# Performance work log

Measured on AMD Instinct MI355X. Metric: run time of the kernel, lower is better.

## Reference

```python
import jax, jax.numpy as jnp
import numpy as np

D_MODEL, D_INNER, D_STATE, DT_RANK, D_CONV = 1024, 2048, 16, 64, 4
B, L = 2, 2048


def setup_inputs() -> dict:
    key = jax.random.key(0)
    ks = jax.random.split(key, 14)
    s = lambda k, shp, fan: jax.random.normal(k, shp, jnp.float32) / np.sqrt(fan)
    return {
        "resid": jax.random.normal(ks[0], (B, L, D_MODEL), jnp.float32),
        "norm_w": jnp.ones((D_MODEL,), jnp.float32),
        "skip_w": s(ks[1], (D_INNER, D_MODEL), D_MODEL),
        "in_w": s(ks[2], (D_INNER, D_MODEL), D_MODEL),
        "conv_w": s(ks[3], (D_INNER, D_CONV), D_CONV),
        "conv_b": jnp.zeros((D_INNER,), jnp.float32),
        "wd1": s(ks[4], (DT_RANK, D_INNER), D_INNER),
        "wd2": s(ks[5], (D_INNER, DT_RANK), DT_RANK),
        "wd2_b": jnp.zeros((D_INNER,), jnp.float32),
        "wb": s(ks[6], (D_STATE, D_INNER), D_INNER),
        "wc": s(ks[7], (D_STATE, D_INNER), D_INNER),
        "A_log": jax.random.normal(ks[8], (D_INNER, D_STATE), jnp.float32),
        "W_D": jnp.ones((D_INNER,), jnp.float32),
        "out_w": s(ks[9], (D_MODEL, D_INNER), D_INNER),
    }


def _rmsnorm(x, w, eps=1e-5):
    return x * jax.lax.rsqrt(jnp.mean(x * x, axis=-1, keepdims=True) + eps) * w


def _causal_depthwise_conv(x, conv_w, conv_b):
    # x: (B, L, E); conv_w: (E, K). Torch Conv1d padding=K-1 then slice [:L] == causal left pad.
    K = conv_w.shape[1]
    xp = jnp.pad(x, ((0, 0), (K - 1, 0), (0, 0)))
    Lx = x.shape[1]
    out = conv_b
    for k in range(K):
        out = out + xp[:, k:k + Lx, :] * conv_w[:, k]
    return out


def _selective_scan(x, delta, Bm, Cm, A):
    # x, delta: (B, L, E); Bm, Cm: (B, L, N); A: (E, N)
    h0 = jnp.zeros((x.shape[0], A.shape[0], A.shape[1]), x.dtype)

    def step(h, inp):
        xt, dt, bt, ct = inp  # (B,E), (B,E), (B,N), (B,N)
        A_bar = jnp.exp(dt[..., None] * A)                      # (B,E,N)
        h = A_bar * h + (dt * xt)[..., None] * bt[:, None, :]   # (B,E,N)
        y = jnp.einsum('ben,bn->be', h, ct)
        return h, y

    xs = tuple(jnp.swapaxes(a, 0, 1) for a in (x, delta, Bm, Cm))
    _, ys = jax.lax.scan(step, h0, xs)
    return jnp.swapaxes(ys, 0, 1)  # (B, L, E)


def reference(resid, norm_w, skip_w, in_w, conv_w, conv_b, wd1, wd2, wd2_b, wb, wc, A_log, W_D, out_w):
    x = _rmsnorm(resid, norm_w)
    skip = x @ skip_w.T                       # (B,L,E)
    x = x @ in_w.T                            # (B,L,E)
    x = _causal_depthwise_conv(x, conv_w, conv_b)
    x = jax.nn.silu(x)
    A = -jnp.exp(A_log)                       # (E,N)
    delta = jax.nn.softplus((x @ wd1.T) @ wd2.T + wd2_b)  # (B,L,E)
    Bm = x @ wb.T                             # (B,L,N)
    Cm = x @ wc.T                             # (B,L,N)
    y = _selective_scan(x, delta, Bm, Cm, A)
    y = y + x * W_D
    y = y * jax.nn.silu(skip)
    y = y @ out_w.T                           # (B,L,D)
    return resid + y
```

## Files before the change

kernel.cpp:

```cpp
#include <hip/hip_runtime.h>
#include <stdint.h>

typedef unsigned short u16;
typedef unsigned int u32;
typedef __bf16 bf16x8 __attribute__((ext_vector_type(8)));
typedef u16 u16x8 __attribute__((ext_vector_type(8)));
typedef float f32x4 __attribute__((ext_vector_type(4)));

#define LOG2E 1.44269504088896340736f

__device__ __forceinline__ u16 f2bf(float f) {
  u32 u = __float_as_uint(f);
  u += 0x7fffu + ((u >> 16) & 1u);
  return (u16)(u >> 16);
}
__device__ __forceinline__ float bf2f(u16 s) { return __uint_as_float(((u32)s) << 16); }
__device__ __forceinline__ float fexp2(float x) { return __builtin_amdgcn_exp2f(x); }

struct alignas(8) U16x4 { u16 x, y, z, w; };

__device__ __forceinline__ void load_lds16(const u16* g, u16* l) {
  __builtin_amdgcn_global_load_lds((const __attribute__((address_space(1))) void*)g,
                                   (__attribute__((address_space(3))) void*)l, 16, 0, 0);
}

struct CvtArgs {
  const float* src[8];
  u16* dst[8];
  int cnt4[8];
  int total4;
};

__global__ __launch_bounds__(256) void cvt8_kernel(CvtArgs a) {
  for (int g = blockIdx.x * 256 + threadIdx.x; g < a.total4; g += gridDim.x * 256) {
    int i = 0, off = g;
    while (off >= a.cnt4[i]) { off -= a.cnt4[i]; ++i; }
    float4 v = make_float4(0.f, 0.f, 0.f, 0.f);
    if (a.src[i]) v = ((const float4*)a.src[i])[off];
    U16x4 o;
    o.x = f2bf(v.x); o.y = f2bf(v.y); o.z = f2bf(v.z); o.w = f2bf(v.w);
    ((U16x4*)a.dst[i])[off] = o;
  }
}

__global__ __launch_bounds__(256) void cvt_t96_kernel(const float* __restrict__ src,
                                                      u16* __restrict__ dst) {
  const int g = blockIdx.x * 256 + threadIdx.x;
  const float4 v = ((const float4*)src)[g];
  U16x4 o;
  o.x = f2bf(v.x); o.y = f2bf(v.y); o.z = f2bf(v.z); o.w = f2bf(v.w);
  ((U16x4*)dst)[g] = o;
}

__global__ __launch_bounds__(256) void rmsnorm_kernel(const float* __restrict__ resid,
                                                      const float* __restrict__ w,
                                                      u16* __restrict__ xn) {
  const int row = blockIdx.x;
  const int tid = threadIdx.x;
  const float4 v = ((const float4*)(resid + (size_t)row * 1024))[tid];
  float ss = v.x * v.x + v.y * v.y + v.z * v.z + v.w * v.w;
#pragma unroll
  for (int off = 32; off > 0; off >>= 1) ss += __shfl_down(ss, off, 64);
  __shared__ float red[4];
  const int lane = tid & 63, wid = tid >> 6;
  if (lane == 0) red[wid] = ss;
  __syncthreads();
  const float tot = red[0] + red[1] + red[2] + red[3];
  const float sc = rsqrtf(tot * (1.0f / 1024.0f) + 1e-5f);
  const float4 wv = ((const float4*)w)[tid];
  U16x4 o;
  o.x = f2bf(v.x * sc * wv.x); o.y = f2bf(v.y * sc * wv.y);
  o.z = f2bf(v.z * sc * wv.z); o.w = f2bf(v.w * sc * wv.w);
  ((U16x4*)(xn + (size_t)row * 1024))[tid] = o;
}

template <int EPI>
__global__ __launch_bounds__(256) void gemm_bt(
    const u16* __restrict__ A, const u16* __restrict__ Bw,
    void* __restrict__ C1, void* __restrict__ C2,
    const float* __restrict__ bias, const float* __restrict__ resid,
    int Kslice, int lda, int ldb, int ldc, int split, int nstore) {
  __shared__ alignas(16) u16 As[2][128 * 32];
  __shared__ alignas(16) u16 Bs[2][128 * 32];
  const int tid = threadIdx.x;
  const int lane = tid & 63, wid = tid >> 6;
  const int wr = wid >> 1, wcid = wid & 1;

  int bx, by;
  {
    const int gy = gridDim.y;
    const int flat = blockIdx.y * 32 + blockIdx.x;
    if ((gy & 3) == 0) {
      const int xcd = flat & 7, idx = flat >> 3;
      const int sy = gy >> 2;
      bx = (xcd & 1) * 16 + (idx & 15);
      by = (xcd >> 1) * sy + (idx >> 4);
    } else { bx = blockIdx.x; by = blockIdx.y; }
  }

  const long brow = (long)bx * 128, bcol = (long)by * 128;
  const int kt0 = blockIdx.z * Kslice;
  const int nt = Kslice >> 5;

  f32x4 acc[4][4] = {};

  const int srow = tid >> 2;
  const int scol = ((tid & 3) ^ ((srow >> 1) & 3)) * 8;
  const u16* Ag = A + (brow + srow) * (long)lda + scol;
  const u16* Bg = Bw + (bcol + srow) * (long)ldb + scol;
  const int fr = lane & 15;
  const int kk2 = ((lane >> 4) ^ ((lane >> 1) & 3)) * 8;

  {
    u16* Asp = As[0] + tid * 8;
    u16* Bsp = Bs[0] + tid * 8;
    load_lds16(Ag + kt0, Asp);
    load_lds16(Ag + kt0 + 64L * lda, Asp + 64 * 32);
    load_lds16(Bg + kt0, Bsp);
    load_lds16(Bg + kt0 + 64L * ldb, Bsp + 64 * 32);
  }
  __syncthreads();

  int cur = 0;
  for (int t = 0; t < nt; ++t) {
    if (t + 1 < nt) {
      const int kt = kt0 + (t + 1) * 32;
      u16* Asp = As[cur ^ 1] + tid * 8;
      u16* Bsp = Bs[cur ^ 1] + tid * 8;
      load_lds16(Ag + kt, Asp);
      load_lds16(Ag + kt + 64L * lda, Asp + 64 * 32);
      load_lds16(Bg + kt, Bsp);
      load_lds16(Bg + kt + 64L * ldb, Bsp + 64 * 32);
    }
    bf16x8 af[4], bfr[4];
#pragma unroll
    for (int i = 0; i < 4; ++i) {
      af[i]  = *(const bf16x8*)(As[cur] + (wr * 64 + i * 16 + fr) * 32 + kk2);
      bfr[i] = *(const bf16x8*)(Bs[cur] + (wcid * 64 + i * 16 + fr) * 32 + kk2);
    }
#pragma unroll
    for (int i = 0; i < 4; ++i)
#pragma unroll
      for (int j = 0; j < 4; ++j)
        acc[i][j] = __builtin_amdgcn_mfma_f32_16x16x32_bf16(af[i], bfr[j], acc[i][j], 0, 0, 0);
    if (t + 1 < nt) __syncthreads();
    cur ^= 1;
  }

  const int fq = lane >> 4;
#pragma unroll
  for (int i = 0; i < 4; ++i) {
#pragma unroll
    for (int j = 0; j < 4; ++j) {
      const long col = bcol + wcid * 64 + j * 16 + fr;
      if ((int)col < nstore) {
#pragma unroll
        for (int r = 0; r < 4; ++r) {
          const long row = brow + wr * 64 + i * 16 + fq * 4 + r;
          float v = acc[i][j][r];
          if (EPI == 1) {
            v += bias[col];
            v = fmaxf(v, 0.f) + log1pf(__expf(-fabsf(v)));
          }
          if (EPI == 4) {
            atomicAdd((float*)C1 + row * ldc + col, v);
          } else if (EPI == 2) {
            ((float*)C1)[row * ldc + col] = v + resid[row * ldc + col];
          } else if ((int)col < split) {
            ((u16*)C1)[row * ldc + col] = f2bf(v);
          } else {
            ((u16*)C2)[row * ldc + (col - split)] = f2bf(v);
          }
        }
      }
    }
  }
}

__global__ __launch_bounds__(256) void conv_silu_kernel(
    const u16* __restrict__ u, const float* __restrict__ cw, const float* __restrict__ cb,
    u16* __restrict__ xc) {
  const int row = blockIdx.x;
  const int l = row & 2047;
  const int t = threadIdx.x;
  const int e0 = t * 8;
  const size_t base = (size_t)row * 2048 + e0;
  bf16x8 xv[4];
#pragma unroll
  for (int k = 0; k < 4; ++k) {
    const int ls = l - 3 + k;
    if (ls >= 0) xv[k] = *(const bf16x8*)(u + base + (long)(k - 3) * 2048);
    else { bf16x8 z = {}; xv[k] = z; }
  }
  u16x8 o;
#pragma unroll
  for (int j = 0; j < 8; ++j) {
    const int e = e0 + j;
    const float4 w = ((const float4*)cw)[e];
    float acc = cb[e];
    acc = fmaf(w.x, (float)xv[0][j], acc);
    acc = fmaf(w.y, (float)xv[1][j], acc);
    acc = fmaf(w.z, (float)xv[2][j], acc);
    acc = fmaf(w.w, (float)xv[3][j], acc);
    const float s = acc / (1.f + __expf(-acc));
    o[j] = f2bf(s);
  }
  *(u16x8*)(xc + base) = o;
}

__global__ __launch_bounds__(256) void scan_p1(
    const u16* __restrict__ delta, const u16* __restrict__ xc, const u16* __restrict__ t96,
    const float* __restrict__ A_log, float* __restrict__ P, float* __restrict__ H) {
  const int tid = threadIdx.x;
  const int e = blockIdx.x * 256 + tid;
  const int c = blockIdx.y, b = blockIdx.z;
  __shared__ alignas(16) u16 Dsh[32 * 256];
  __shared__ alignas(16) u16 Xsh[32 * 256];
  __shared__ float Bsh[32][16];
  const size_t rowbase = ((size_t)(b * 2048 + c * 32)) * 2048 + blockIdx.x * 256;
#pragma unroll
  for (int k = 0; k < 4; ++k) {
    const int i = tid + k * 256;
    const size_t go = rowbase + (size_t)(i >> 5) * 2048 + (i & 31) * 8;
    load_lds16(delta + go, Dsh + i * 8);
    load_lds16(xc + go, Xsh + i * 8);
  }
  for (int i = tid; i < 512; i += 256) {
    const int l0 = i >> 4, n = i & 15;
    Bsh[l0][n] = bf2f(t96[(size_t)(b * 2048 + c * 32 + l0) * 96 + 64 + n]);
  }
  float kv[16], h[16];
#pragma unroll
  for (int n = 0; n < 16; ++n) {
    kv[n] = -__expf(A_log[(size_t)e * 16 + n]) * LOG2E;
    h[n] = 0.f;
  }
  __syncthreads();
  float sdt = 0.f;
  for (int l0 = 0; l0 < 32; ++l0) {
    const float dt = bf2f(Dsh[l0 * 256 + tid]);
    const float x  = bf2f(Xsh[l0 * 256 + tid]);
    const float dtx = dt * x;
    sdt += dt;
#pragma unroll
    for (int n = 0; n < 16; ++n) {
      const float ab = fexp2(kv[n] * dt);
      h[n] = fmaf(ab, h[n], dtx * Bsh[l0][n]);
    }
  }
  const size_t o0 = (((size_t)(b * 64 + c)) * 16) * 2048 + e;
#pragma unroll
  for (int n = 0; n < 16; ++n) {
    P[o0 + (size_t)n * 2048] = fexp2(kv[n] * sdt);
    H[o0 + (size_t)n * 2048] = h[n];
  }
}

__global__ __launch_bounds__(256) void scan_p2(float* __restrict__ P, float* __restrict__ H) {
  const int g = blockIdx.x * 256 + threadIdx.x;
  const int e = g & 2047;
  const int n = (g >> 11) & 15;
  const int b = g >> 15;
  const size_t base = (((size_t)(b * 64)) * 16 + n) * 2048 + e;
  float h = 0.f;
  for (int c = 0; c < 64; ++c) {
    const size_t a = base + (size_t)c * (16 * 2048);
    const float Pc = P[a], hl = H[a];
    H[a] = h;
    h = fmaf(Pc, h, hl);
  }
}

__global__ __launch_bounds__(256) void scan_p3(
    const u16* __restrict__ delta, const u16* __restrict__ xc, const u16* __restrict__ t96,
    const float* __restrict__ A_log, const float* __restrict__ Hin,
    const u16* __restrict__ skip, const float* __restrict__ W_D, u16* __restrict__ ybar) {
  const int tid = threadIdx.x;
  const int e = blockIdx.x * 256 + tid;
  const int c = blockIdx.y, b = blockIdx.z;
  __shared__ alignas(16) u16 Dsh[32 * 256];
  __shared__ alignas(16) u16 Xsh[32 * 256];
  __shared__ float Bsh[32][16], Csh[32][16];
  const size_t rowbase = ((size_t)(b * 2048 + c * 32)) * 2048 + blockIdx.x * 256;
#pragma unroll
  for (int k = 0; k < 4; ++k) {
    const int i = tid + k * 256;
    const size_t go = rowbase + (size_t)(i >> 5) * 2048 + (i & 31) * 8;
    load_lds16(delta + go, Dsh + i * 8);
    load_lds16(xc + go, Xsh + i * 8);
  }
  for (int i = tid; i < 512; i += 256) {
    const int l0 = i >> 4, n = i & 15;
    const size_t rowo = (size_t)(b * 2048 + c * 32 + l0) * 96;
    Bsh[l0][n] = bf2f(t96[rowo + 64 + n]);
    Csh[l0][n] = bf2f(t96[rowo + 80 + n]);
  }
  float kv[16], h[16];
  const size_t o0 = (((size_t)(b * 64 + c)) * 16) * 2048 + e;
#pragma unroll
  for (int n = 0; n < 16; ++n) {
    kv[n] = -__expf(A_log[(size_t)e * 16 + n]) * LOG2E;
    h[n] = Hin[o0 + (size_t)n * 2048];
  }
  const float wd = W_D[e];
  __syncthreads();
  const size_t base = ((size_t)(b * 2048 + c * 32)) * 2048 + e;
  for (int l0 = 0; l0 < 32; ++l0) {
    const float dt = bf2f(Dsh[l0 * 256 + tid]);
    const float x  = bf2f(Xsh[l0 * 256 + tid]);
    const float dtx = dt * x;
    float y = 0.f;
#pragma unroll
    for (int n = 0; n < 16; ++n) {
      const float ab = fexp2(kv[n] * dt);
      h[n] = fmaf(ab, h[n], dtx * Bsh[l0][n]);
      y = fmaf(h[n], Csh[l0][n], y);
    }
    y = fmaf(x, wd, y);
    const float s = bf2f(skip[base + (size_t)l0 * 2048]);
    y *= s / (1.f + __expf(-s));
    ybar[base + (size_t)l0 * 2048] = f2bf(y);
  }
}

extern "C" void kernel_launch(void* const* d_in, const int* in_sizes, int n_in,
                              void* d_out, int out_size, void* d_ws, size_t ws_size,
                              hipStream_t stream) {
  const float* resid  = (const float*)d_in[0];
  const float* norm_w = (const float*)d_in[1];
  const float* skip_w = (const float*)d_in[2];
  const float* in_w   = (const float*)d_in[3];
  const float* conv_w = (const float*)d_in[4];
  const float* conv_b = (const float*)d_in[5];
  const float* wd1    = (const float*)d_in[6];
  const float* wd2    = (const float*)d_in[7];
  const float* wd2_b  = (const float*)d_in[8];
  const float* wb     = (const float*)d_in[9];
  const float* wc     = (const float*)d_in[10];
  const float* A_log  = (const float*)d_in[11];
  const float* W_D    = (const float*)d_in[12];
  const float* out_w  = (const float*)d_in[13];
  float* out = (float*)d_out;

  char* ws = (char*)d_ws;
  u16* w_in   = (u16*)(ws + 0);
  u16* w_skip = (u16*)(ws + 4194304);
  u16* w_out  = (u16*)(ws + 8388608);
  u16* w_wd2  = (u16*)(ws + 12582912);
  u16* w2cat  = (u16*)(ws + 12845056);
  u16* xn     = (u16*)(ws + 13369344);
  u16* u      = (u16*)(ws + 21757952);
  u16* delta  = u;
  u16* skip   = (u16*)(ws + 38535168);
  u16* xc     = (u16*)(ws + 55312384);
  u16* t96    = (u16*)(ws + 72089600);
  float* P    = (float*)(ws + 72876032);
  float* t96f = (float*)(ws + 72876032);
  u16* ybar   = (u16*)(ws + 72876032);
  float* H    = (float*)(ws + 89653248);

  CvtArgs ca{};
  ca.src[0] = in_w;   ca.dst[0] = w_in;              ca.cnt4[0] = 2097152 / 4;
  ca.src[1] = skip_w; ca.dst[1] = w_skip;            ca.cnt4[1] = 2097152 / 4;
  ca.src[2] = out_w;  ca.dst[2] = w_out;             ca.cnt4[2] = 2097152 / 4;
  ca.src[3] = wd2;    ca.dst[3] = w_wd2;             ca.cnt4[3] = 131072 / 4;
  ca.src[4] = wd1;    ca.dst[4] = w2cat;             ca.cnt4[4] = 131072 / 4;
  ca.src[5] = wb;     ca.dst[5] = w2cat + 64 * 2048; ca.cnt4[5] = 32768 / 4;
  ca.src[6] = wc;     ca.dst[6] = w2cat + 80 * 2048; ca.cnt4[6] = 32768 / 4;
  ca.src[7] = nullptr;ca.dst[7] = w2cat + 96 * 2048; ca.cnt4[7] = 65536 / 4;
  ca.total4 = (2097152 * 3 + 131072 * 2 + 32768 * 2 + 65536) / 4;
  cvt8_kernel<<<2048, 256, 0, stream>>>(ca);

  rmsnorm_kernel<<<4096, 256, 0, stream>>>(resid, norm_w, xn);

  gemm_bt<0><<<dim3(32, 32), 256, 0, stream>>>(xn, w_in, u, skip, nullptr, nullptr,
                                               1024, 1024, 1024, 2048, 2048, 4096);

  conv_silu_kernel<<<4096, 256, 0, stream>>>(u, conv_w, conv_b, xc);

  hipMemsetAsync(t96f, 0, 4096 * 96 * 4, stream);
  gemm_bt<4><<<dim3(32, 1, 4), 256, 0, stream>>>(xc, w2cat, t96f, nullptr, nullptr, nullptr,
                                                 512, 2048, 2048, 96, 1 << 30, 96);
  cvt_t96_kernel<<<384, 256, 0, stream>>>(t96f, t96);

  gemm_bt<1><<<dim3(32, 16), 256, 0, stream>>>(t96, w_wd2, delta, nullptr, wd2_b, nullptr,
                                               64, 96, 64, 2048, 1 << 30, 2048);

  scan_p1<<<dim3(8, 64, 2), 256, 0, stream>>>(delta, xc, t96, A_log, P, H);
  scan_p2<<<256, 256, 0, stream>>>(P, H);
  scan_p3<<<dim3(8, 64, 2), 256, 0, stream>>>(delta, xc, t96, A_log, H, skip, W_D, ybar);

  gemm_bt<2><<<dim3(32, 8), 256, 0, stream>>>(ybar, w_out, out, nullptr, nullptr, resid,
                                              2048, 2048, 2048, 1024, 1 << 30, 1024);
}
```

Baseline: 345.0 us.

## Double GEMM K-tile to 64 with new LDS swizzle and fuse prep kernels

The bf16 GEMM now stages a 64-wide K slice per iteration instead of 32. It uses an 8-chunk XOR swizzle and issues two MFMA sub-steps per barrier, which halves the number of sync/load rounds. The weight conversion and RMSNorm kernels are merged into one launch that splits work by block index, saving a launch and letting both run concurrently. The cost is double the LDS per block (64KB), which may lower occupancy.

```diff
diff --git a/kernel.cpp b/kernel.cpp
--- a/kernel.cpp
+++ b/kernel.cpp
@@ -31,15 +31,38 @@
   int total4;
 };
 
-__global__ __launch_bounds__(256) void cvt8_kernel(CvtArgs a) {
-  for (int g = blockIdx.x * 256 + threadIdx.x; g < a.total4; g += gridDim.x * 256) {
-    int i = 0, off = g;
-    while (off >= a.cnt4[i]) { off -= a.cnt4[i]; ++i; }
-    float4 v = make_float4(0.f, 0.f, 0.f, 0.f);
-    if (a.src[i]) v = ((const float4*)a.src[i])[off];
+__global__ __launch_bounds__(256) void prep_kernel(CvtArgs a,
+                                                   const float* __restrict__ resid,
+                                                   const float* __restrict__ w,
+                                                   u16* __restrict__ xn) {
+  const int tid = threadIdx.x;
+  if (blockIdx.x < 4096) {
+    const int row = blockIdx.x;
+    const float4 v = ((const float4*)(resid + (size_t)row * 1024))[tid];
+    float ss = v.x * v.x + v.y * v.y + v.z * v.z + v.w * v.w;
+#pragma unroll
+    for (int off = 32; off > 0; off >>= 1) ss += __shfl_down(ss, off, 64);
+    __shared__ float red[4];
+    const int lane = tid & 63, wid = tid >> 6;
+    if (lane == 0) red[wid] = ss;
+    __syncthreads();
+    const float tot = red[0] + red[1] + red[2] + red[3];
+    const float sc = rsqrtf(tot * (1.0f / 1024.0f) + 1e-5f);
+    const float4 wv = ((const float4*)w)[tid];
     U16x4 o;
-    o.x = f2bf(v.x); o.y = f2bf(v.y); o.z = f2bf(v.z); o.w = f2bf(v.w);
-    ((U16x4*)a.dst[i])[off] = o;
+    o.x = f2bf(v.x * sc * wv.x); o.y = f2bf(v.y * sc * wv.y);
+    o.z = f2bf(v.z * sc * wv.z); o.w = f2bf(v.w * sc * wv.w);
+    ((U16x4*)(xn + (size_t)row * 1024))[tid] = o;
+  } else {
+    for (int g = (blockIdx.x - 4096) * 256 + tid; g < a.total4; g += 2048 * 256) {
+      int i = 0, off = g;
+      while (off >= a.cnt4[i]) { off -= a.cnt4[i]; ++i; }
+      float4 v = make_float4(0.f, 0.f, 0.f, 0.f);
+      if (a.src[i]) v = ((const float4*)a.src[i])[off];
+      U16x4 o;
+      o.x = f2bf(v.x); o.y = f2bf(v.y); o.z = f2bf(v.z); o.w = f2bf(v.w);
+      ((U16x4*)a.dst[i])[off] = o;
+    }
   }
 }
 
@@ -52,36 +75,14 @@
   ((U16x4*)dst)[g] = o;
 }
 
-__global__ __launch_bounds__(256) void rmsnorm_kernel(const float* __restrict__ resid,
-                                                      const float* __restrict__ w,
-                                                      u16* __restrict__ xn) {
-  const int row = blockIdx.x;
-  const int tid = threadIdx.x;
-  const float4 v = ((const float4*)(resid + (size_t)row * 1024))[tid];
-  float ss = v.x * v.x + v.y * v.y + v.z * v.z + v.w * v.w;
-#pragma unroll
-  for (int off = 32; off > 0; off >>= 1) ss += __shfl_down(ss, off, 64);
-  __shared__ float red[4];
-  const int lane = tid & 63, wid = tid >> 6;
-  if (lane == 0) red[wid] = ss;
-  __syncthreads();
-  const float tot = red[0] + red[1] + red[2] + red[3];
-  const float sc = rsqrtf(tot * (1.0f / 1024.0f) + 1e-5f);
-  const float4 wv = ((const float4*)w)[tid];
-  U16x4 o;
-  o.x = f2bf(v.x * sc * wv.x); o.y = f2bf(v.y * sc * wv.y);
-  o.z = f2bf(v.z * sc * wv.z); o.w = f2bf(v.w * sc * wv.w);
-  ((U16x4*)(xn + (size_t)row * 1024))[tid] = o;
-}
-
 template <int EPI>
 __global__ __launch_bounds__(256) void gemm_bt(
     const u16* __restrict__ A, const u16* __restrict__ Bw,
     void* __restrict__ C1, void* __restrict__ C2,
     const float* __restrict__ bias, const float* __restrict__ resid,
     int Kslice, int lda, int ldb, int ldc, int split, int nstore) {
-  __shared__ alignas(16) u16 As[2][128 * 32];
-  __shared__ alignas(16) u16 Bs[2][128 * 32];
+  __shared__ alignas(16) u16 As[2][128 * 64];
+  __shared__ alignas(16) u16 Bs[2][128 * 64];
   const int tid = threadIdx.x;
   const int lane = tid & 63, wid = tid >> 6;
   const int wr = wid >> 1, wcid = wid & 1;
@@ -100,54 +101,54 @@
 
   const long brow = (long)bx * 128, bcol = (long)by * 128;
   const int kt0 = blockIdx.z * Kslice;
-  const int nt = Kslice >> 5;
+  const int nt = Kslice >> 6;
 
   f32x4 acc[4][4] = {};
 
-  const int srow = tid >> 2;
-  const int scol = ((tid & 3) ^ ((srow >> 1) & 3)) * 8;
+  const int srow = tid >> 3;
+  const int scol = ((tid & 7) ^ (srow & 7)) * 8;
   const u16* Ag = A + (brow + srow) * (long)lda + scol;
   const u16* Bg = Bw + (bcol + srow) * (long)ldb + scol;
   const int fr = lane & 15;
-  const int kk2 = ((lane >> 4) ^ ((lane >> 1) & 3)) * 8;
-
-  {
-    u16* Asp = As[0] + tid * 8;
-    u16* Bsp = Bs[0] + tid * 8;
-    load_lds16(Ag + kt0, Asp);
-    load_lds16(Ag + kt0 + 64L * lda, Asp + 64 * 32);
-    load_lds16(Bg + kt0, Bsp);
-    load_lds16(Bg + kt0 + 64L * ldb, Bsp + 64 * 32);
-  }
+  const int fq = lane >> 4;
+  const int ck0 = ((fq) ^ (fr & 7)) * 8;
+  const int ck1 = ((4 + fq) ^ (fr & 7)) * 8;
+
+  auto stage = [&](int buf, int kt) {
+    u16* Asp = As[buf] + tid * 8;
+    u16* Bsp = Bs[buf] + tid * 8;
+#pragma unroll
+    for (int kq = 0; kq < 4; ++kq) {
+      load_lds16(Ag + kt + (long)(kq * 32) * lda, Asp + kq * 2048);
+      load_lds16(Bg + kt + (long)(kq * 32) * ldb, Bsp + kq * 2048);
+    }
+  };
+
+  stage(0, kt0);
   __syncthreads();
 
   int cur = 0;
   for (int t = 0; t < nt; ++t) {
-    if (t + 1 < nt) {
-      const int kt = kt0 + (t + 1) * 32;
-      u16* Asp = As[cur ^ 1] + tid * 8;
-      u16* Bsp = Bs[cur ^ 1] + tid * 8;
-      load_lds16(Ag + kt, Asp);
-      load_lds16(Ag + kt + 64L * lda, Asp + 64 * 32);
-      load_lds16(Bg + kt, Bsp);
-      load_lds16(Bg + kt + 64L * ldb, Bsp + 64 * 32);
-    }
-    bf16x8 af[4], bfr[4];
-#pragma unroll
-    for (int i = 0; i < 4; ++i) {
-      af[i]  = *(const bf16x8*)(As[cur] + (wr * 64 + i * 16 + fr) * 32 + kk2);
-      bfr[i] = *(const bf16x8*)(Bs[cur] + (wcid * 64 + i * 16 + fr) * 32 + kk2);
-    }
-#pragma unroll
-    for (int i = 0; i < 4; ++i)
-#pragma unroll
-      for (int j = 0; j < 4; ++j)
-        acc[i][j] = __builtin_amdgcn_mfma_f32_16x16x32_bf16(af[i], bfr[j], acc[i][j], 0, 0, 0);
+    if (t + 1 < nt) stage(cur ^ 1, kt0 + (t + 1) * 64);
+#pragma unroll
+    for (int ks = 0; ks < 2; ++ks) {
+      const int ck = ks ? ck1 : ck0;
+      bf16x8 af[4], bfr[4];
+#pragma unroll
+      for (int i = 0; i < 4; ++i) {
+        af[i]  = *(const bf16x8*)(As[cur] + (wr * 64 + i * 16 + fr) * 64 + ck);
+        bfr[i] = *(const bf16x8*)(Bs[cur] + (wcid * 64 + i * 16 + fr) * 64 + ck);
+      }
+#pragma unroll
+      for (int i = 0; i < 4; ++i)
+#pragma unroll
+        for (int j = 0; j < 4; ++j)
+          acc[i][j] = __builtin_amdgcn_mfma_f32_16x16x32_bf16(af[i], bfr[j], acc[i][j], 0, 0, 0);
+    }
     if (t + 1 < nt) __syncthreads();
     cur ^= 1;
   }
 
-  const int fq = lane >> 4;
 #pragma unroll
   for (int i = 0; i < 4; ++i) {
 #pragma unroll
@@ -369,9 +370,8 @@
   ca.src[6] = wc;     ca.dst[6] = w2cat + 80 * 2048; ca.cnt4[6] = 32768 / 4;
   ca.src[7] = nullptr;ca.dst[7] = w2cat + 96 * 2048; ca.cnt4[7] = 65536 / 4;
   ca.total4 = (2097152 * 3 + 131072 * 2 + 32768 * 2 + 65536) / 4;
-  cvt8_kernel<<<2048, 256, 0, stream>>>(ca);
-
-  rmsnorm_kernel<<<4096, 256, 0, stream>>>(resid, norm_w, xn);
+
+  prep_kernel<<<6144, 256, 0, stream>>>(ca, resid, norm_w, xn);
 
   gemm_bt<0><<<dim3(32, 32), 256, 0, stream>>>(xn, w_in, u, skip, nullptr, nullptr,
                                                1024, 1024, 1024, 2048, 2048, 4096);
```

After: 327.2 us. -5.2%, faster.
